# Kernel optimization log

Hardware: AMD Instinct MI355X
Metric: run time of the kernel (lower is better)

Reference implementation:

```python
import jax, jax.numpy as jnp
import numpy as np

BATCH_SIZE = 4096
N_VIEWS = 2
NUM_GPU = 1
TEMPERATURE = 0.07
FEAT_DIM = 128
N = (BATCH_SIZE // NUM_GPU) * N_VIEWS  # 8192


def setup_inputs() -> dict:
    key = jax.random.key(0)
    features = jax.random.normal(key, (N, FEAT_DIM), dtype=jnp.float32)
    return {"features": features}


def reference(features):
    n = features.shape[0]
    b = BATCH_SIZE // NUM_GPU
    # labels: [arange(b)] * n_views concatenated -> pairwise equality matrix
    lbl_vec = jnp.tile(jnp.arange(b), N_VIEWS)            # [N]
    lab = lbl_vec[None, :] == lbl_vec[:, None]            # [N, N] bool

    # F.normalize(dim=1): divide by L2 norm clamped at 1e-12
    norm = jnp.linalg.norm(features, axis=1, keepdims=True)
    f = features / jnp.maximum(norm, 1e-12)
    sim = f @ f.T                                          # [N, N]

    # Remove diagonal: row i keeps columns j != i in original order.
    cols = jnp.arange(n - 1)
    off_idx = cols[None, :] + (cols[None, :] >= jnp.arange(n)[:, None])  # [N, N-1]
    sim_od = jnp.take_along_axis(sim, off_idx, axis=1)     # [N, N-1]
    lab_od = jnp.take_along_axis(lab, off_idx, axis=1)     # [N, N-1] bool

    # Stable sort: positives (label True) first, preserving original column order,
    # matching torch's masked-select + concat([positives, negatives]).
    order = jnp.argsort(~lab_od, axis=1, stable=True)      # [N, N-1]
    logits = jnp.take_along_axis(sim_od, order, axis=1) / TEMPERATURE

    # CrossEntropyLoss with target class 0 (mean reduction)
    loss = -jax.nn.log_softmax(logits, axis=1)[:, 0]
    return loss.mean()
```

## Files before the change

kernel.cpp:

```cpp
#include <hip/hip_runtime.h>
#include <hip/hip_bf16.h>
#include <cstdint>

#define NROWS 8192
#define FDIM  128
#define HALF_N 4096

typedef short bf16x8 __attribute__((ext_vector_type(8)));
typedef float f32x4  __attribute__((ext_vector_type(4)));

#define K1 (1.4426950408889634f / 0.07f)

#if __has_builtin(__builtin_amdgcn_exp2f)
#define EXP2(x) __builtin_amdgcn_exp2f(x)
#else
#define EXP2(x) exp2f(x)
#endif


__global__ void __launch_bounds__(256) normalize_kernel(const float* __restrict__ f,
                                                        short* __restrict__ packed,
                                                        float* __restrict__ esum_g) {
    const int row  = blockIdx.x * 4 + (threadIdx.x >> 6);
    const int lane = threadIdx.x & 63;
    const float2 v = ((const float2*)(f + (size_t)row * FDIM))[lane];
    float ss = v.x * v.x + v.y * v.y;
    #pragma unroll
    for (int m = 1; m < 64; m <<= 1) ss += __shfl_xor(ss, m);
    const float scale = 1.0f / fmaxf(sqrtf(ss), 1e-12f);

    const int off = ((((row >> 4) * 4 + (lane >> 4)) * 64)
                     + ((lane >> 2) & 3) * 16 + (row & 15)) * 8 + 2 * (lane & 3);
    __hip_bfloat16 b0 = __float2bfloat16(v.x * scale);
    __hip_bfloat16 b1 = __float2bfloat16(v.y * scale);
    unsigned u = (unsigned)*(unsigned short*)&b0
               | ((unsigned)*(unsigned short*)&b1 << 16);
    *(unsigned*)(packed + off) = u;

    if (threadIdx.x < 4) esum_g[blockIdx.x * 4 + threadIdx.x] = 0.0f;
}

__device__ __forceinline__ float2 bf2_to_f2(unsigned u) {
    return make_float2(__uint_as_float(u << 16),
                       __uint_as_float(u & 0xffff0000u));
}

__global__ void __launch_bounds__(256, 3) sim_kernel(const short* __restrict__ pk,
                                                     float* __restrict__ esum_g,
                                                     float* __restrict__ pos_g,
                                                     float* __restrict__ diag_g) {
    if (blockIdx.x >= 512) {
        const int i  = (blockIdx.x - 512) * 256 + threadIdx.x;
        const int ip = i ^ HALF_N;
        const uint4* P = (const uint4*)pk;
        float dot = 0.f, self = 0.f;
        #pragma unroll
        for (int c = 0; c < 16; c++) {
            const uint4 a = P[((i  >> 4) * 4 + (c >> 2)) * 64 + (c & 3) * 16 + (i  & 15)];
            const uint4 b = P[((ip >> 4) * 4 + (c >> 2)) * 64 + (c & 3) * 16 + (ip & 15)];
            const unsigned au[4] = {a.x, a.y, a.z, a.w};
            const unsigned bu[4] = {b.x, b.y, b.z, b.w};
            #pragma unroll
            for (int q = 0; q < 4; q++) {
                const float2 av = bf2_to_f2(au[q]);
                const float2 bv = bf2_to_f2(bu[q]);
                dot  = __builtin_fmaf(av.x, bv.x, __builtin_fmaf(av.y, bv.y, dot));
                self = __builtin_fmaf(av.x, av.x, __builtin_fmaf(av.y, av.y, self));
            }
        }
        pos_g[i]  = dot;
        diag_g[i] = EXP2(__builtin_fmaf(self, K1, -K1));
        return;
    }

    const int tid   = threadIdx.x;
    const int w     = tid >> 6;
    const int lane  = tid & 63;
    const int j     = blockIdx.x & 15;
    const int strip = (blockIdx.x >> 4) * 4 + w;
    const bf16x8* P = (const bf16x8*)pk;

    bf16x8 a_reg[4][4];
    #pragma unroll
    for (int fr = 0; fr < 4; fr++)
        #pragma unroll
        for (int ks = 0; ks < 4; ks++)
            a_reg[ks][fr] = P[((strip * 4 + fr) * 4 + ks) * 64 + lane];

    float ep[4][4];
    #pragma unroll
    for (int a = 0; a < 4; a++)
        #pragma unroll
        for (int b = 0; b < 4; b++) ep[a][b] = 0.0f;

    const int cb0 = j * 32;
    bf16x8 b0[4], b1[4];
    #pragma unroll
    for (int ks = 0; ks < 4; ks++)
        b0[ks] = P[(cb0 * 4 + ks) * 64 + lane];

#define COMPUTE(BF)                                                          \
    {                                                                        \
        f32x4 acc[4];                                                        \
        _Pragma("unroll")                                                    \
        for (int fr = 0; fr < 4; fr++) acc[fr] = (f32x4){0.f, 0.f, 0.f, 0.f};\
        _Pragma("unroll")                                                    \
        for (int ks = 0; ks < 4; ks++)                                       \
            _Pragma("unroll")                                                \
            for (int fr = 0; fr < 4; fr++)                                   \
                acc[fr] = __builtin_amdgcn_mfma_f32_16x16x32_bf16(           \
                              a_reg[ks][fr], BF[ks], acc[fr], 0, 0, 0);      \
        _Pragma("unroll")                                                    \
        for (int fr = 0; fr < 4; fr++)                                       \
            _Pragma("unroll")                                                \
            for (int r = 0; r < 4; r++)                                      \
                ep[fr][r] += EXP2(__builtin_fmaf(acc[fr][r], K1, -K1));      \
    }

    for (int cb = 0; cb < 32; cb += 2) {
        #pragma unroll
        for (int ks = 0; ks < 4; ks++)
            b1[ks] = P[((cb0 + cb + 1) * 4 + ks) * 64 + lane];
        COMPUTE(b0);
        if (cb + 2 < 32) {
            #pragma unroll
            for (int ks = 0; ks < 4; ks++)
                b0[ks] = P[((cb0 + cb + 2) * 4 + ks) * 64 + lane];
        }
        COMPUTE(b1);
    }
#undef COMPUTE

    #pragma unroll
    for (int fr = 0; fr < 4; fr++)
        #pragma unroll
        for (int r = 0; r < 4; r++) {
            float v = ep[fr][r];
            #pragma unroll
            for (int m = 1; m < 16; m <<= 1) v += __shfl_xor(v, m);
            if ((lane & 15) == 0)
                atomicAdd(&esum_g[strip * 64 + fr * 16 + (lane >> 4) * 4 + r], v);
        }
}

__global__ void __launch_bounds__(256) final_kernel(const float* __restrict__ esum_g,
                                                    const float* __restrict__ pos_g,
                                                    const float* __restrict__ diag_g,
                                                    float* __restrict__ out) {
    const int tid = threadIdx.x;
    const float invT = 1.0f / 0.07f;
    float acc = 0.0f;
    for (int i = tid; i < NROWS; i += 256)
        acc += logf(esum_g[i] - diag_g[i]) + invT - pos_g[i] * invT;
    #pragma unroll
    for (int m = 1; m < 64; m <<= 1) acc += __shfl_xor(acc, m);
    __shared__ float ws[4];
    if ((tid & 63) == 0) ws[tid >> 6] = acc;
    __syncthreads();
    if (tid == 0) out[0] = (ws[0] + ws[1] + ws[2] + ws[3]) * (1.0f / (float)NROWS);
}

extern "C" void kernel_launch(void* const* d_in, const int* in_sizes, int n_in,
                              void* d_out, int out_size, void* d_ws, size_t ws_size,
                              hipStream_t stream) {
    const float* features = (const float*)d_in[0];
    float* out = (float*)d_out;

    char* ws = (char*)d_ws;
    short* packed = (short*)ws;
    float* esum_g = (float*)(ws + (size_t)NROWS * FDIM * 2);
    float* pos_g  = (float*)(ws + (size_t)NROWS * FDIM * 2 + NROWS * 4);
    float* diag_g = (float*)(ws + (size_t)NROWS * FDIM * 2 + NROWS * 8);

    normalize_kernel<<<NROWS / 4, 256, 0, stream>>>(features, packed, esum_g);

    sim_kernel<<<512 + NROWS / 256, 256, 0, stream>>>(packed, esum_g, pos_g, diag_g);

    final_kernel<<<1, 256, 0, stream>>>(esum_g, pos_g, diag_g, out);
}
```

Baseline: 89.16 us.

## Exploit similarity matrix symmetry to compute only upper-triangle tiles

The similarity tile loop now covers only about half of the 64-row strip pairs. Each computed off-diagonal tile adds its exp sums to the row strip and, through column sums reduced with shuffles and atomics, to the partner strip, so roughly half the MFMA and exp work is removed. Work is split into 260 column-tile units per strip, spread over 16 waves with triple-buffered B loads, and launch bounds drop occupancy from 3 to 2 blocks per CU. The cost is many more global atomics, imbalanced waves (some handle 17 units, some 16), and possible register-pressure or occupancy changes.

```diff
diff --git a/kernel.cpp b/kernel.cpp
--- a/kernel.cpp
+++ b/kernel.cpp
@@ -45,7 +45,7 @@
                        __uint_as_float(u & 0xffff0000u));
 }
 
-__global__ void __launch_bounds__(256, 3) sim_kernel(const short* __restrict__ pk,
+__global__ void __launch_bounds__(256, 2) sim_kernel(const short* __restrict__ pk,
                                                      float* __restrict__ esum_g,
                                                      float* __restrict__ pos_g,
                                                      float* __restrict__ diag_g) {
@@ -55,9 +55,9 @@
         const uint4* P = (const uint4*)pk;
         float dot = 0.f, self = 0.f;
         #pragma unroll
-        for (int c = 0; c < 16; c++) {
-            const uint4 a = P[((i  >> 4) * 4 + (c >> 2)) * 64 + (c & 3) * 16 + (i  & 15)];
-            const uint4 b = P[((ip >> 4) * 4 + (c >> 2)) * 64 + (c & 3) * 16 + (ip & 15)];
+        for (int cc = 0; cc < 16; cc++) {
+            const uint4 a = P[((i  >> 4) * 4 + (cc >> 2)) * 64 + (cc & 3) * 16 + (i  & 15)];
+            const uint4 b = P[((ip >> 4) * 4 + (cc >> 2)) * 64 + (cc & 3) * 16 + (ip & 15)];
             const unsigned au[4] = {a.x, a.y, a.z, a.w};
             const unsigned bu[4] = {b.x, b.y, b.z, b.w};
             #pragma unroll
@@ -76,8 +76,10 @@
     const int tid   = threadIdx.x;
     const int w     = tid >> 6;
     const int lane  = tid & 63;
-    const int j     = blockIdx.x & 15;
-    const int strip = (blockIdx.x >> 4) * 4 + w;
+    const int quad  = lane >> 4;
+    const int l16   = lane & 15;
+    const int strip = blockIdx.x >> 2;
+    const int c     = (blockIdx.x & 3) * 4 + w;
     const bf16x8* P = (const bf16x8*)pk;
 
     bf16x8 a_reg[4][4];
@@ -93,43 +95,64 @@
         #pragma unroll
         for (int b = 0; b < 4; b++) ep[a][b] = 0.0f;
 
-    const int cb0 = j * 32;
-    bf16x8 b0[4], b1[4];
-    #pragma unroll
-    for (int ks = 0; ks < 4; ks++)
-        b0[ks] = P[(cb0 * 4 + ks) * 64 + lane];
-
-#define COMPUTE(BF)                                                          \
-    {                                                                        \
-        f32x4 acc[4];                                                        \
-        _Pragma("unroll")                                                    \
-        for (int fr = 0; fr < 4; fr++) acc[fr] = (f32x4){0.f, 0.f, 0.f, 0.f};\
-        _Pragma("unroll")                                                    \
-        for (int ks = 0; ks < 4; ks++)                                       \
-            _Pragma("unroll")                                                \
-            for (int fr = 0; fr < 4; fr++)                                   \
-                acc[fr] = __builtin_amdgcn_mfma_f32_16x16x32_bf16(           \
-                              a_reg[ks][fr], BF[ks], acc[fr], 0, 0, 0);      \
-        _Pragma("unroll")                                                    \
-        for (int fr = 0; fr < 4; fr++)                                       \
-            _Pragma("unroll")                                                \
-            for (int r = 0; r < 4; r++)                                      \
-                ep[fr][r] += EXP2(__builtin_fmaf(acc[fr][r], K1, -K1));      \
+    auto cb_clamp = [&](int p) { return (p < 260) ? p : c; };
+    auto cb_base  = [&](int p) {
+        const int d = p >> 2, fc = p & 3;
+        const int js = (strip + d) & 127;
+        return ((js * 4 + fc) * 4) * 64 + lane;
+    };
+
+    bf16x8 bbuf[3][4];
+    {
+        const int b0 = cb_base(cb_clamp(c));
+        const int b1 = cb_base(cb_clamp(c + 16));
+        #pragma unroll
+        for (int ks = 0; ks < 4; ks++) {
+            bbuf[0][ks] = P[b0 + ks * 64];
+            bbuf[1][ks] = P[b1 + ks * 64];
+        }
     }
 
-    for (int cb = 0; cb < 32; cb += 2) {
-        #pragma unroll
-        for (int ks = 0; ks < 4; ks++)
-            b1[ks] = P[((cb0 + cb + 1) * 4 + ks) * 64 + lane];
-        COMPUTE(b0);
-        if (cb + 2 < 32) {
+    #pragma unroll
+    for (int k = 0; k < 17; k++) {
+        if (k + 2 < 17) {
+            const int bn = cb_base(cb_clamp(c + 16 * (k + 2)));
             #pragma unroll
             for (int ks = 0; ks < 4; ks++)
-                b0[ks] = P[((cb0 + cb + 2) * 4 + ks) * 64 + lane];
-        }
-        COMPUTE(b1);
+                bbuf[(k + 2) % 3][ks] = P[bn + ks * 64];
+        }
+        const int p = c + 16 * k;
+        if (p < 260) {
+            const int d  = p >> 2, fc = p & 3;
+            const int js = (strip + d) & 127;
+
+            f32x4 acc[4];
+            #pragma unroll
+            for (int fr = 0; fr < 4; fr++) acc[fr] = (f32x4){0.f, 0.f, 0.f, 0.f};
+            #pragma unroll
+            for (int ks = 0; ks < 4; ks++)
+                #pragma unroll
+                for (int fr = 0; fr < 4; fr++)
+                    acc[fr] = __builtin_amdgcn_mfma_f32_16x16x32_bf16(
+                                  a_reg[ks][fr], bbuf[k % 3][ks], acc[fr], 0, 0, 0);
+
+            float cs = 0.0f;
+            #pragma unroll
+            for (int fr = 0; fr < 4; fr++)
+                #pragma unroll
+                for (int r = 0; r < 4; r++) {
+                    const float e = EXP2(__builtin_fmaf(acc[fr][r], K1, -K1));
+                    ep[fr][r] += e;
+                    cs += e;
+                }
+            if (d != 0 && d != 64) {
+                cs += __shfl_xor(cs, 16);
+                cs += __shfl_xor(cs, 32);
+                if (lane < 16)
+                    atomicAdd(&esum_g[js * 64 + fc * 16 + lane], cs);
+            }
+        }
     }
-#undef COMPUTE
 
     #pragma unroll
     for (int fr = 0; fr < 4; fr++)
@@ -138,8 +161,8 @@
             float v = ep[fr][r];
             #pragma unroll
             for (int m = 1; m < 16; m <<= 1) v += __shfl_xor(v, m);
-            if ((lane & 15) == 0)
-                atomicAdd(&esum_g[strip * 64 + fr * 16 + (lane >> 4) * 4 + r], v);
+            if (l16 == 0)
+                atomicAdd(&esum_g[strip * 64 + fr * 16 + quad * 4 + r], v);
         }
 }
 
```

Result: slower. 107.3 us (+20.3%).
